# Kernel tuning notes

Hardware: AMD Instinct MI355X
Metric: run time of the kernel (lower is better)

Reference implementation:

```python
import jax, jax.numpy as jnp
import numpy as np

N_ATOMS = 100000
M_NBRS = 12
ATOM_F = 64
NBR_F = 41
BN_EPS = 1e-5


def setup_inputs() -> dict:
    key = jax.random.key(0)
    k1, k2, k3, k4, k5 = jax.random.split(key, 5)
    atom_fea = jax.random.normal(k1, (N_ATOMS, ATOM_F), dtype=jnp.float32)
    nbr_fea = jax.random.normal(k2, (N_ATOMS, M_NBRS, NBR_F), dtype=jnp.float32)
    # fc_full: Linear(2*atom + nbr -> 2*atom), torch layout [out, in]
    in_dim = 2 * ATOM_F + NBR_F
    out_dim = 2 * ATOM_F
    W = jax.random.normal(k3, (out_dim, in_dim), dtype=jnp.float32) * (1.0 / np.sqrt(in_dim))
    b = jax.random.normal(k4, (out_dim,), dtype=jnp.float32) * 0.01
    gamma = jnp.ones((ATOM_F,), dtype=jnp.float32)
    beta = jnp.zeros((ATOM_F,), dtype=jnp.float32)
    nbr_idx = jax.random.randint(k5, (N_ATOMS, M_NBRS), 0, N_ATOMS, dtype=jnp.int32)
    return {"atom_fea": atom_fea, "nbr_fea": nbr_fea, "W": W, "b": b,
            "gamma": gamma, "beta": beta, "nbr_idx": nbr_idx}


def reference(atom_fea, nbr_fea, W, b, gamma, beta, nbr_idx):
    N, M = nbr_idx.shape
    F = atom_fea.shape[1]
    # gather neighbor atom features: [N, M, F]
    nbr_atom_fea = atom_fea[nbr_idx]
    # broadcast self features: [N, M, F]
    self_fea = jnp.broadcast_to(atom_fea[:, None, :], (N, M, F))
    # concat [self, nbr_atom, edge] -> [N, M, 2F + nbr_F]
    total_fea = jnp.concatenate([self_fea, nbr_atom_fea, nbr_fea], axis=2)
    # shared linear: [N, M, 2F]
    total_fea = jnp.einsum('nmi,oi->nmo', total_fea, W) + b
    filter_fea, core_fea = jnp.split(total_fea, 2, axis=2)
    # gated message, sum over neighbors -> [N, F]
    nbr_msg = (jax.nn.sigmoid(filter_fea) * jax.nn.softplus(core_fea)).sum(axis=1)
    # BatchNorm1d (training mode: batch stats, biased variance)
    x = atom_fea + nbr_msg
    mean = x.mean(axis=0)
    var = x.var(axis=0)
    x_hat = (x - mean) * jax.lax.rsqrt(var + BN_EPS)
    out = x_hat * gamma + beta
    return jax.nn.softplus(out)
```

## Files before the change

### kernel.cpp

```cpp
#include <hip/hip_runtime.h>
#include <hip/hip_bf16.h>

#define N_ATOMS 100000
#define M_NBRS 12
#define ATOM_F 64
#define NBR_F 41
#define OUT_DIM 128
#define IN_DIM 169

typedef __attribute__((ext_vector_type(8))) short short8;
typedef __attribute__((ext_vector_type(4))) float f32x4;

__device__ __forceinline__ unsigned short f2bf(float f) {
    union { float f; unsigned u; } v; v.f = f;
    unsigned u = v.u;
    return (unsigned short)((u + 0x7fffu + ((u >> 16) & 1u)) >> 16);
}
__device__ __forceinline__ float bf2f(unsigned short h) {
    union { unsigned u; float f; } v; v.u = ((unsigned)h) << 16;
    return v.f;
}
__device__ __forceinline__ unsigned pack_bf2(float lo, float hi) {
    return (unsigned)f2bf(lo) | (((unsigned)f2bf(hi)) << 16);
}
__device__ __forceinline__ float softplus_f(float x) {
    return fmaxf(x, 0.f) + __logf(1.f + __expf(-fabsf(x)));
}
__device__ __forceinline__ float sigmoid_f(float x) {
    return 1.f / (1.f + __expf(-x));
}

#define WS_STRIDE 72
__global__ __launch_bounds__(256, 4) void k_prep(
    const float* __restrict__ atom, const float* __restrict__ W,
    const float* __restrict__ bias, unsigned* __restrict__ abf_u32,
    unsigned* __restrict__ A1u_out)
{
    __shared__ unsigned short Ws[128 * WS_STRIDE];
    __shared__ unsigned Ap[4 * 16 * 36];
    __shared__ unsigned short T1[4][16 * 136];
    const int tid = threadIdx.x;
    const int w = tid >> 6, l = tid & 63;
    const int r = l & 15, g = l >> 4;

    for (int e = tid; e < 128 * 64; e += 256) {
        int col = e >> 6, k = e & 63;
        Ws[col * WS_STRIDE + k] = f2bf(W[col * IN_DIM + k]);
    }
    __syncthreads();

    short8 bf[8][2];
    #pragma unroll
    for (int nt = 0; nt < 8; ++nt)
      #pragma unroll
      for (int kk = 0; kk < 2; ++kk) {
            int col = nt * 16 + r;
            union { uint4 u; short8 s; } u;
            u.u = *reinterpret_cast<const uint4*>(&Ws[col * WS_STRIDE + kk * 32 + g * 8]);
            bf[nt][kk] = u.s;
      }

    float bb[8];
    #pragma unroll
    for (int nt = 0; nt < 8; ++nt) bb[nt] = bias[nt * 16 + r];

    const int totalw = gridDim.x * 4;
    const int gw = blockIdx.x * 4 + w;
    const int step = totalw * 16;
    const int T = (N_ATOMS + step - 1) / step;
    unsigned* Aw = &Ap[w * 16 * 36];
    unsigned short* Tw = T1[w];

    for (int t = 0; t < T; ++t) {
        int base = gw * 16 + t * step;
        #pragma unroll
        for (int sub = 0; sub < 4; ++sub) {
            int chunk = g * 4 + sub;
            int a = base + r;
            float4 v = make_float4(0.f, 0.f, 0.f, 0.f);
            if (a < N_ATOMS)
                v = reinterpret_cast<const float4*>(atom)[a * 16 + chunk];
            Aw[r * 36 + chunk * 2]     = pack_bf2(v.x, v.y);
            Aw[r * 36 + chunk * 2 + 1] = pack_bf2(v.z, v.w);
        }
        {
            int al = l >> 2, part = l & 3;
            int a = base + al;
            if (a < N_ATOMS) {
                uint4 d0 = *reinterpret_cast<const uint4*>(&Aw[al * 36 + part * 8]);
                uint4 d1 = *reinterpret_cast<const uint4*>(&Aw[al * 36 + part * 8 + 4]);
                reinterpret_cast<uint4*>(&abf_u32[a * 32 + part * 8])[0] = d0;
                reinterpret_cast<uint4*>(&abf_u32[a * 32 + part * 8 + 4])[0] = d1;
            }
        }
        short8 af[2];
        #pragma unroll
        for (int kk = 0; kk < 2; ++kk) {
            union { uint4 u; short8 s; } u;
            u.u = *reinterpret_cast<const uint4*>(&Aw[r * 36 + kk * 16 + g * 4]);
            af[kk] = u.s;
        }
        #pragma unroll
        for (int nt = 0; nt < 8; ++nt) {
            f32x4 acc = {0.f, 0.f, 0.f, 0.f};
            acc = __builtin_amdgcn_mfma_f32_16x16x32_bf16(af[0], bf[nt][0], acc, 0, 0, 0);
            acc = __builtin_amdgcn_mfma_f32_16x16x32_bf16(af[1], bf[nt][1], acc, 0, 0, 0);
            int col = nt * 16 + r;
            #pragma unroll
            for (int r4 = 0; r4 < 4; ++r4) {
                int al = g * 4 + r4;
                Tw[al * 136 + col] = f2bf(acc[r4] + bb[nt]);
            }
        }
        {
            int al = l >> 2, part = l & 3;
            int a = base + al;
            if (a < N_ATOMS) {
                const unsigned* Twu = reinterpret_cast<const unsigned*>(&Tw[al * 136]);
                #pragma unroll
                for (int q = 0; q < 4; ++q) {
                    uint4 d = *reinterpret_cast<const uint4*>(&Twu[part * 16 + q * 4]);
                    reinterpret_cast<uint4*>(&A1u_out[a * 64 + part * 16 + q * 4])[0] = d;
                }
            }
        }
    }
}

struct Buf {
    unsigned ga[3], gb[3];
    float e0[3], e1[3], e2[3], e3[3];
    unsigned a1v;
    float av;
};

__device__ __forceinline__ Buf issue_loads(
    int i, bool act, unsigned idxv,
    const unsigned* __restrict__ abf_u32, const float* __restrict__ nbr,
    const unsigned* __restrict__ A1u, const float* __restrict__ atom,
    int c, int g, int l)
{
    Buf b;
    if (act) {
        #pragma unroll
        for (int rr = 0; rr < 3; ++rr) {
            int r = rr * 4 + g;
            int j = (int)__shfl(idxv, r, 64);
            b.ga[rr] = abf_u32[j * 32 + c];
            b.gb[rr] = abf_u32[j * 32 + 16 + c];
            int eb = (i * M_NBRS + r) * NBR_F;
            b.e0[rr] = nbr[eb + 2 * c];
            b.e1[rr] = nbr[eb + 2 * c + 1];
            b.e2[rr] = (c < 5) ? nbr[eb + 32 + 2 * c] : 0.f;
            b.e3[rr] = (c < 4) ? nbr[eb + 33 + 2 * c] : 0.f;
        }
        b.a1v = A1u[i * 64 + l];
        b.av  = atom[i * 64 + l];
    } else {
        #pragma unroll
        for (int rr = 0; rr < 3; ++rr) {
            b.ga[rr] = b.gb[rr] = 0u;
            b.e0[rr] = b.e1[rr] = b.e2[rr] = b.e3[rr] = 0.f;
        }
        b.a1v = 0u; b.av = 0.f;
    }
    return b;
}

#define BS_STRIDE 136
__global__ __launch_bounds__(256, 2) void k_msg(
    const float* __restrict__ atom, const float* __restrict__ nbr,
    const float* __restrict__ W, const int* __restrict__ idx,
    const unsigned* __restrict__ abf_u32, const unsigned* __restrict__ A1u,
    float* __restrict__ X)
{
    __shared__ unsigned short Bs[128 * BS_STRIDE];
    __shared__ unsigned Au[4 * 16 * 68];
    const int tid = threadIdx.x;
    const int w = tid >> 6, l = tid & 63;
    const int c = l & 15, g = l >> 4;
    unsigned* Aw = &Au[w * 16 * 68];

    for (int e = tid; e < 128 * BS_STRIDE / 2; e += 256)
        reinterpret_cast<unsigned*>(Bs)[e] = 0u;
    __syncthreads();
    for (int e = tid; e < 128 * 105; e += 256) {
        unsigned col = (unsigned)e / 105u;
        unsigned k = (unsigned)e - col * 105u;
        Bs[col * BS_STRIDE + k] = f2bf(W[col * IN_DIM + 64 + k]);
    }
    __syncthreads();

    short8 bf[8][4];
    #pragma unroll
    for (int nt = 0; nt < 8; ++nt)
      #pragma unroll
      for (int kk = 0; kk < 4; ++kk) {
            int col = nt * 16 + c;
            union { uint4 u; short8 s; } u;
            u.u = *reinterpret_cast<const uint4*>(&Bs[col * BS_STRIDE + kk * 32 + g * 8]);
            bf[nt][kk] = u.s;
      }

    for (int t = l; t < 4 * 68; t += 64)
        Aw[12 * 68 + t] = 0u;

    const int TW = gridDim.x * 4;
    const int gw = blockIdx.x * 4 + w;
    const int T = (N_ATOMS + TW - 1) / TW;

    int i0 = gw;
    bool act0 = (i0 < N_ATOMS);
    unsigned idxv0 = (l < 12 && act0) ? (unsigned)idx[i0 * M_NBRS + l] : 0u;
    Buf buf = issue_loads(i0, act0, idxv0, abf_u32, nbr, A1u, atom, c, g, l);
    int i1 = gw + TW;
    unsigned idxv_n = (l < 12 && i1 < N_ATOMS) ? (unsigned)idx[i1 * M_NBRS + l] : 0u;

    for (int t = 0; t < T; ++t) {
        int i = gw + t * TW;
        bool act = (i < N_ATOMS);
        int i_nxt = i + TW;
        bool act_n = (i_nxt < N_ATOMS);

        Buf buf_n = issue_loads(i_nxt, act_n, idxv_n, abf_u32, nbr, A1u, atom, c, g, l);
        int i_n2 = i + 2 * TW;
        unsigned idxv_n2 = (l < 12 && i_n2 < N_ATOMS) ? (unsigned)idx[i_n2 * M_NBRS + l] : 0u;

        if (act) {
            #pragma unroll
            for (int rr = 0; rr < 3; ++rr) {
                int r = rr * 4 + g;
                Aw[r * 68 + c]      = buf.ga[rr];
                Aw[r * 68 + 16 + c] = buf.gb[rr];
                Aw[r * 68 + 32 + c] = pack_bf2(buf.e0[rr], buf.e1[rr]);
                Aw[r * 68 + 48 + c] = (c < 5) ? pack_bf2(buf.e2[rr], buf.e3[rr]) : 0u;
            }
            short8 af[4];
            #pragma unroll
            for (int kk = 0; kk < 4; ++kk) {
                union { uint4 u; short8 s; } u;
                u.u = *reinterpret_cast<const uint4*>(&Aw[c * 68 + kk * 16 + g * 4]);
                af[kk] = u.s;
            }
            #pragma unroll
            for (int p = 0; p < 4; ++p) {
                f32x4 accf = {0.f,0.f,0.f,0.f}, accc = {0.f,0.f,0.f,0.f};
                #pragma unroll
                for (int kk = 0; kk < 4; ++kk) {
                    accf = __builtin_amdgcn_mfma_f32_16x16x32_bf16(af[kk], bf[p][kk],     accf, 0,0,0);
                    accc = __builtin_amdgcn_mfma_f32_16x16x32_bf16(af[kk], bf[p + 4][kk], accc, 0,0,0);
                }
                unsigned a1p = __shfl(buf.a1v, p * 8 + (c >> 1), 64);
                unsigned a1q = __shfl(buf.a1v, 32 + p * 8 + (c >> 1), 64);
                float a1f = bf2f((unsigned short)((c & 1) ? (a1p >> 16) : (a1p & 0xffffu)));
                float a1c = bf2f((unsigned short)((c & 1) ? (a1q >> 16) : (a1q & 0xffffu)));
                float ac  = __shfl(buf.av, p * 16 + c, 64);
                float gs = 0.f;
                if (g < 3) {
                    #pragma unroll
                    for (int r4 = 0; r4 < 4; ++r4) {
                        float zf = accf[r4] + a1f;
                        float zc = accc[r4] + a1c;
                        gs += sigmoid_f(zf) * softplus_f(zc);
                    }
                }
                gs += __shfl_xor(gs, 16, 64);
                gs += __shfl_xor(gs, 32, 64);
                if (g == 0)
                    X[i * ATOM_F + p * 16 + c] = ac + gs;
            }
        }
        buf = buf_n;
        idxv_n = idxv_n2;
    }
}

#define S1_BLOCKS 256
__global__ void k_stats1(const float* __restrict__ X, float* __restrict__ PART)
{
    __shared__ float s1[256], s2[256];
    int tid = threadIdx.x;
    int f = tid & 63;
    int seg = blockIdx.x * 4 + (tid >> 6);
    float sum = 0.f, sq = 0.f;
    for (int a = seg; a < N_ATOMS; a += S1_BLOCKS * 4) {
        float x = X[a * ATOM_F + f];
        sum += x; sq += x * x;
    }
    s1[tid] = sum; s2[tid] = sq;
    __syncthreads();
    if (tid < 64) {
        PART[blockIdx.x * 128 + tid] = s1[tid] + s1[tid+64] + s1[tid+128] + s1[tid+192];
    } else if (tid < 128) {
        int ff = tid - 64;
        PART[blockIdx.x * 128 + tid] = s2[ff] + s2[ff+64] + s2[ff+128] + s2[ff+192];
    }
}

__global__ void k_stats2(const float* __restrict__ PART, const float* __restrict__ gamma,
                         const float* __restrict__ beta, float* __restrict__ MS)
{
    __shared__ float st[128];
    int t = threadIdx.x;
    float s = 0.f;
    #pragma unroll 8
    for (int b = 0; b < S1_BLOCKS; ++b) s += PART[b * 128 + t];
    st[t] = s;
    __syncthreads();
    if (t < 64) {
        float mean = st[t] * (1.f / N_ATOMS);
        float msq  = st[64 + t] * (1.f / N_ATOMS);
        float var  = msq - mean * mean;
        float inv  = rsqrtf(var + 1e-5f);
        float sc   = inv * gamma[t];
        float sh   = beta[t] - mean * sc;
        MS[t] = sc;
        MS[64 + t] = sh;
    }
}

__global__ void k_final(float* __restrict__ X, const float* __restrict__ MS)
{
    int q = blockIdx.x * 256 + threadIdx.x;
    const float4* MS4 = reinterpret_cast<const float4*>(MS);
    float4 x = reinterpret_cast<const float4*>(X)[q];
    float4 sc = MS4[q & 15];
    float4 sh = MS4[16 + (q & 15)];
    float4 o;
    o.x = softplus_f(x.x * sc.x + sh.x);
    o.y = softplus_f(x.y * sc.y + sh.y);
    o.z = softplus_f(x.z * sc.z + sh.z);
    o.w = softplus_f(x.w * sc.w + sh.w);
    reinterpret_cast<float4*>(X)[q] = o;
}

extern "C" void kernel_launch(void* const* d_in, const int* in_sizes, int n_in,
                              void* d_out, int out_size, void* d_ws, size_t ws_size,
                              hipStream_t stream)
{
    const float* atom  = (const float*)d_in[0];
    const float* nbr   = (const float*)d_in[1];
    const float* W     = (const float*)d_in[2];
    const float* bias  = (const float*)d_in[3];
    const float* gamma = (const float*)d_in[4];
    const float* beta  = (const float*)d_in[5];
    const int*   idx   = (const int*)d_in[6];
    float* X = (float*)d_out;

    char* ws = (char*)d_ws;
    unsigned* abf = (unsigned*)ws;
    unsigned* A1u = (unsigned*)(ws + (size_t)N_ATOMS * 64 * 2);
    float* PART   = (float*)(ws + (size_t)N_ATOMS * 64 * 2
                                + (size_t)N_ATOMS * 128 * 2);
    float* MS     = PART + S1_BLOCKS * 128;

    hipLaunchKernelGGL(k_prep,   dim3(512),       dim3(256), 0, stream, atom, W, bias, abf, A1u);
    hipLaunchKernelGGL(k_msg,    dim3(512),       dim3(256), 0, stream, atom, nbr, W, idx, abf, A1u, X);
    hipLaunchKernelGGL(k_stats1, dim3(S1_BLOCKS), dim3(256), 0, stream, X, PART);
    hipLaunchKernelGGL(k_stats2, dim3(1),         dim3(128), 0, stream, PART, gamma, beta, MS);
    hipLaunchKernelGGL(k_final,  dim3(6250),      dim3(256), 0, stream, X, MS);
}
```

Before: 492.5 us.

## Fuse BatchNorm statistics into message kernel and raise occupancy via shared-memory aliasing

Each wave now accumulates per-feature sum and sum of squares while writing X, then adds them into a global buffer with atomics. This removes the separate stats kernel and its full re-read of X. Shared memory for the weight tile and the per-wave A buffer is aliased behind an added barrier, so launch bounds rise to 4 blocks per CU and the grid doubles to 1024. The trade-offs are float atomics, which make the summation order nondeterministic, more register pressure from the higher occupancy target, and an extra memset launch.

```diff
diff --git a/kernel.cpp b/kernel.cpp
--- a/kernel.cpp
+++ b/kernel.cpp
@@ -168,14 +168,16 @@
 }
 
 #define BS_STRIDE 136
-__global__ __launch_bounds__(256, 2) void k_msg(
+__global__ __launch_bounds__(256, 4) void k_msg(
     const float* __restrict__ atom, const float* __restrict__ nbr,
     const float* __restrict__ W, const int* __restrict__ idx,
     const unsigned* __restrict__ abf_u32, const unsigned* __restrict__ A1u,
-    float* __restrict__ X)
-{
-    __shared__ unsigned short Bs[128 * BS_STRIDE];
-    __shared__ unsigned Au[4 * 16 * 68];
+    float* __restrict__ X, float* __restrict__ SSUM)
+{
+    __shared__ char smem[128 * BS_STRIDE * 2];
+    unsigned short* Bs = reinterpret_cast<unsigned short*>(smem);
+    unsigned* Au = reinterpret_cast<unsigned*>(smem);
+
     const int tid = threadIdx.x;
     const int w = tid >> 6, l = tid & 63;
     const int c = l & 15, g = l >> 4;
@@ -201,6 +203,7 @@
             u.u = *reinterpret_cast<const uint4*>(&Bs[col * BS_STRIDE + kk * 32 + g * 8]);
             bf[nt][kk] = u.s;
       }
+    __syncthreads();
 
     for (int t = l; t < 4 * 68; t += 64)
         Aw[12 * 68 + t] = 0u;
@@ -208,6 +211,9 @@
     const int TW = gridDim.x * 4;
     const int gw = blockIdx.x * 4 + w;
     const int T = (N_ATOMS + TW - 1) / TW;
+
+    float zsum[4] = {0.f, 0.f, 0.f, 0.f};
+    float zsq[4]  = {0.f, 0.f, 0.f, 0.f};
 
     int i0 = gw;
     bool act0 = (i0 < N_ATOMS);
@@ -266,50 +272,34 @@
                 }
                 gs += __shfl_xor(gs, 16, 64);
                 gs += __shfl_xor(gs, 32, 64);
-                if (g == 0)
-                    X[i * ATOM_F + p * 16 + c] = ac + gs;
+                if (g == 0) {
+                    float xv = ac + gs;
+                    X[i * ATOM_F + p * 16 + c] = xv;
+                    zsum[p] += xv;
+                    zsq[p]  += xv * xv;
+                }
             }
         }
         buf = buf_n;
         idxv_n = idxv_n2;
     }
-}
-
-#define S1_BLOCKS 256
-__global__ void k_stats1(const float* __restrict__ X, float* __restrict__ PART)
-{
-    __shared__ float s1[256], s2[256];
-    int tid = threadIdx.x;
-    int f = tid & 63;
-    int seg = blockIdx.x * 4 + (tid >> 6);
-    float sum = 0.f, sq = 0.f;
-    for (int a = seg; a < N_ATOMS; a += S1_BLOCKS * 4) {
-        float x = X[a * ATOM_F + f];
-        sum += x; sq += x * x;
-    }
-    s1[tid] = sum; s2[tid] = sq;
-    __syncthreads();
-    if (tid < 64) {
-        PART[blockIdx.x * 128 + tid] = s1[tid] + s1[tid+64] + s1[tid+128] + s1[tid+192];
-    } else if (tid < 128) {
-        int ff = tid - 64;
-        PART[blockIdx.x * 128 + tid] = s2[ff] + s2[ff+64] + s2[ff+128] + s2[ff+192];
-    }
-}
-
-__global__ void k_stats2(const float* __restrict__ PART, const float* __restrict__ gamma,
+
+    if (g == 0) {
+        #pragma unroll
+        for (int p = 0; p < 4; ++p) {
+            atomicAdd(&SSUM[p * 16 + c], zsum[p]);
+            atomicAdd(&SSUM[64 + p * 16 + c], zsq[p]);
+        }
+    }
+}
+
+__global__ void k_stats2(const float* __restrict__ SSUM, const float* __restrict__ gamma,
                          const float* __restrict__ beta, float* __restrict__ MS)
 {
-    __shared__ float st[128];
     int t = threadIdx.x;
-    float s = 0.f;
-    #pragma unroll 8
-    for (int b = 0; b < S1_BLOCKS; ++b) s += PART[b * 128 + t];
-    st[t] = s;
-    __syncthreads();
     if (t < 64) {
-        float mean = st[t] * (1.f / N_ATOMS);
-        float msq  = st[64 + t] * (1.f / N_ATOMS);
+        float mean = SSUM[t] * (1.f / N_ATOMS);
+        float msq  = SSUM[64 + t] * (1.f / N_ATOMS);
         float var  = msq - mean * mean;
         float inv  = rsqrtf(var + 1e-5f);
         float sc   = inv * gamma[t];
@@ -350,13 +340,13 @@
     char* ws = (char*)d_ws;
     unsigned* abf = (unsigned*)ws;
     unsigned* A1u = (unsigned*)(ws + (size_t)N_ATOMS * 64 * 2);
-    float* PART   = (float*)(ws + (size_t)N_ATOMS * 64 * 2
+    float* SSUM   = (float*)(ws + (size_t)N_ATOMS * 64 * 2
                                 + (size_t)N_ATOMS * 128 * 2);
-    float* MS     = PART + S1_BLOCKS * 128;
-
-    hipLaunchKernelGGL(k_prep,   dim3(512),       dim3(256), 0, stream, atom, W, bias, abf, A1u);
-    hipLaunchKernelGGL(k_msg,    dim3(512),       dim3(256), 0, stream, atom, nbr, W, idx, abf, A1u, X);
-    hipLaunchKernelGGL(k_stats1, dim3(S1_BLOCKS), dim3(256), 0, stream, X, PART);
-    hipLaunchKernelGGL(k_stats2, dim3(1),         dim3(128), 0, stream, PART, gamma, beta, MS);
-    hipLaunchKernelGGL(k_final,  dim3(6250),      dim3(256), 0, stream, X, MS);
-}
+    float* MS     = SSUM + 128;
+
+    hipMemsetAsync(SSUM, 0, 128 * sizeof(float), stream);
+    hipLaunchKernelGGL(k_prep,   dim3(1024), dim3(256), 0, stream, atom, W, bias, abf, A1u);
+    hipLaunchKernelGGL(k_msg,    dim3(1024), dim3(256), 0, stream, atom, nbr, W, idx, abf, A1u, X, SSUM);
+    hipLaunchKernelGGL(k_stats2, dim3(1),    dim3(64),  0, stream, SSUM, gamma, beta, MS);
+    hipLaunchKernelGGL(k_final,  dim3(6250), dim3(256), 0, stream, X, MS);
+}
```

New measurement: 764.2 us. 1.55x slower.
